# Kernel tuning notes

Hardware: AMD Instinct MI355X
Metric: run time of the kernel (lower is better)

The kernel has to match this reference:

```python
import jax, jax.numpy as jnp
import numpy as np

EPS = 1e-5

def _layer_norm(x, gamma, beta):
    mu = jnp.mean(x, axis=-1, keepdims=True)
    var = jnp.mean(jnp.square(x - mu), axis=-1, keepdims=True)
    return (x - mu) * jax.lax.rsqrt(var + EPS) * gamma + beta

def setup_inputs() -> dict:
    key = jax.random.key(0)
    ks = jax.random.split(key, 4)
    B, S, D, F = 4, 2048, 1024, 4096
    return {
        "hidden_state": jax.random.normal(ks[0], (B, S, D), dtype=jnp.float32),
        "attention_mask": jnp.zeros((B, S), dtype=jnp.float32),
        "w1": jax.random.normal(ks[1], (D, F), dtype=jnp.float32) * (1.0 / np.sqrt(D)),
        "b1": jnp.zeros((F,), dtype=jnp.float32),
        "w2": jax.random.normal(ks[2], (F, D), dtype=jnp.float32) * (1.0 / np.sqrt(F)),
        "b2": jnp.zeros((D,), dtype=jnp.float32),
        "ln1_gamma": jnp.ones((D,), dtype=jnp.float32),
        "ln1_beta": jnp.zeros((D,), dtype=jnp.float32),
        "ln2_gamma": jnp.ones((D,), dtype=jnp.float32),
        "ln2_beta": jnp.zeros((D,), dtype=jnp.float32),
    }

def reference(hidden_state, attention_mask, w1, b1, w2, b2,
              ln1_gamma, ln1_beta, ln2_gamma, ln2_beta):
    h = hidden_state
    d = h.shape[-1]
    # Self-attention with Q=K=V=h (no projections), single head.
    scores = jnp.einsum("bqd,bkd->bqk", h, h) / jnp.sqrt(jnp.float32(d))
    scores = scores + attention_mask[:, None, :]  # additive mask [B,1,S]
    probs = jax.nn.softmax(scores, axis=-1)
    attn_out = jnp.einsum("bqk,bkd->bqd", probs, h)
    # Residual + post-LN (dropout inactive in eval)
    h = _layer_norm(h + attn_out, ln1_gamma, ln1_beta)
    # FFN: Linear -> exact GELU -> Linear
    ffn = jax.nn.gelu(h @ w1 + b1, approximate=False) @ w2 + b2
    h = _layer_norm(h + ffn, ln2_gamma, ln2_beta)
    return h
```

## Files before the change

### kernel.cpp

```cpp
#include <hip/hip_runtime.h>
#include <hip/hip_bf16.h>
#include <math.h>

typedef __bf16 bf16;
typedef __bf16 bf16x8 __attribute__((ext_vector_type(8)));
typedef float  f32x4  __attribute__((ext_vector_type(4)));

__device__ __forceinline__ float gelu_f(float x) {
    return 0.5f * x * (1.0f + erff(x * 0.70710678118654752440f));
}

__global__ void detect_k(const unsigned short* __restrict__ h, int* __restrict__ flag)
{
    if (threadIdx.x == 0 && blockIdx.x == 0) {
        int cnt = 0;
        for (int i = 0; i < 256; i += 2) {
            int e = (h[i] >> 7) & 0xFF;
            cnt += (e >= 100 && e <= 140) ? 1 : 0;
        }
        *flag = (cnt >= 96) ? 0 : 1;
    }
}

struct SmallConvArgs {
    const void* src[7];
    bf16* dst[7];
    int n[7];
};
__global__ __launch_bounds__(256) void small_convert_k(SmallConvArgs a,
                                                       const int* __restrict__ flag)
{
    const int seg = blockIdx.y;
    const int i = blockIdx.x * 256 + threadIdx.x;
    if (i >= a.n[seg]) return;
    const float v = (*flag) ? ((const float*)a.src[seg])[i]
                            : (float)((const bf16*)a.src[seg])[i];
    a.dst[seg][i] = (bf16)v;
}

__global__ __launch_bounds__(256) void conv_transpose_k(
    const void* __restrict__ in, bf16* __restrict__ outT,
    int R, int C, const int* __restrict__ flag)
{
    __shared__ bf16 tile[32][33];
    const int c0 = blockIdx.x * 32;
    const int r0 = blockIdx.y * 32;
    const int tx = threadIdx.x & 31;
    const int ty = threadIdx.x >> 5;
    const bool f32 = (*flag) != 0;
#pragma unroll
    for (int i = 0; i < 32; i += 8) {
        const long idx = (long)(r0 + ty + i) * C + (c0 + tx);
        const float v = f32 ? ((const float*)in)[idx] : (float)((const bf16*)in)[idx];
        tile[ty + i][tx] = (bf16)v;
    }
    __syncthreads();
#pragma unroll
    for (int i = 0; i < 32; i += 8)
        outT[(long)(c0 + ty + i) * R + (r0 + tx)] = tile[tx][ty + i];
}

__global__ __launch_bounds__(256) void conv_transpose_h_k(
    const void* __restrict__ in, bf16* __restrict__ h_bf, bf16* __restrict__ hT,
    int S, int D, const int* __restrict__ flag)
{
    __shared__ bf16 tile[32][33];
    const long sB = (long)S * D;
    const int d0 = blockIdx.x * 32;
    const int s0 = blockIdx.y * 32;
    const int b  = blockIdx.z;
    const int tx = threadIdx.x & 31;
    const int ty = threadIdx.x >> 5;
    const bool f32 = (*flag) != 0;
#pragma unroll
    for (int i = 0; i < 32; i += 8) {
        const long idx = b * sB + (long)(s0 + ty + i) * D + (d0 + tx);
        const float v = f32 ? ((const float*)in)[idx] : (float)((const bf16*)in)[idx];
        const bf16 bv = (bf16)v;
        h_bf[idx] = bv;
        tile[ty + i][tx] = bv;
    }
    __syncthreads();
#pragma unroll
    for (int i = 0; i < 32; i += 8)
        hT[b * sB + (long)(d0 + ty + i) * S + (s0 + tx)] = tile[tx][ty + i];
}

__device__ __forceinline__ void gll16(const bf16* g, bf16* l)
{
    __builtin_amdgcn_global_load_lds(
        (const __attribute__((address_space(1))) void*)g,
        (__attribute__((address_space(3))) void*)l, 16, 0, 0);
}

template <int MODE, int STAGE>
__global__ __launch_bounds__(256) void gemm_nt(
    const bf16* __restrict__ A, const bf16* __restrict__ Bt,
    bf16* __restrict__ C, const bf16* __restrict__ bias,
    int M, int N, int K, float scale,
    long sA, long sB, long sC)
{
    A  += (long)blockIdx.z * sA;
    Bt += (long)blockIdx.z * sB;
    C  += (long)blockIdx.z * sC;

    const int tileM = blockIdx.y * 128;
    const int tileN = blockIdx.x * 128;

    const int t    = threadIdx.x;
    const int lane = t & 63;
    const int wave = t >> 6;
    const int wr   = wave >> 1;
    const int wc   = wave & 1;
    const int quad = lane >> 4;
    const int l16  = lane & 15;

    const int srow   = lane >> 3;
    const int lchunk = ((lane & 7) - srow) & 7;

    f32x4 acc[4][4] = {};

    auto swz = [](int row, int chunk) { return row * 64 + (((chunk + row) & 7) * 8); };

    auto stage = [&](bf16* as, bf16* bs, int k0) {
#pragma unroll
        for (int r2 = 0; r2 < 4; ++r2) {
            const int unit = wave * 4 + r2;
            const int row  = unit * 8 + srow;
            const int col  = lchunk * 8;
            gll16(A  + (long)(tileM + row) * K + (k0 + col), as + unit * 512);
            gll16(Bt + (long)(tileN + row) * K + (k0 + col), bs + unit * 512);
        }
    };

    auto compute = [&](const bf16* as, const bf16* bs) {
#pragma unroll
        for (int kk = 0; kk < 64; kk += 32) {
            const int chunk = (kk >> 3) + quad;
            bf16x8 af[4], bfr[4];
#pragma unroll
            for (int i = 0; i < 4; ++i) {
                af[i]  = *(const bf16x8*)&as[swz(wr * 64 + i * 16 + l16, chunk)];
                bfr[i] = *(const bf16x8*)&bs[swz(wc * 64 + i * 16 + l16, chunk)];
            }
#pragma unroll
            for (int mi = 0; mi < 4; ++mi)
#pragma unroll
                for (int ni = 0; ni < 4; ++ni)
                    acc[mi][ni] = __builtin_amdgcn_mfma_f32_16x16x32_bf16(
                        af[mi], bfr[ni], acc[mi][ni], 0, 0, 0);
        }
    };

    if constexpr (STAGE == 2) {
        __shared__ __align__(16) bf16 As0[128 * 64];
        __shared__ __align__(16) bf16 As1[128 * 64];
        __shared__ __align__(16) bf16 Bs0[128 * 64];
        __shared__ __align__(16) bf16 Bs1[128 * 64];

        stage(As0, Bs0, 0);
        __syncthreads();
        for (int u = 0; u < K / 64; u += 2) {
            const int k1 = (u + 1) * 64;
            const int k2 = (u + 2) * 64;
            if (k1 < K) stage(As1, Bs1, k1);
            compute(As0, Bs0);
            __syncthreads();
            if (k1 < K) {
                if (k2 < K) stage(As0, Bs0, k2);
                compute(As1, Bs1);
                __syncthreads();
            }
        }
    } else {
        __shared__ __align__(16) bf16 As[128 * 64];
        __shared__ __align__(16) bf16 Bs[128 * 64];
        for (int k0 = 0; k0 < K; k0 += 64) {
            stage(As, Bs, k0);
            __syncthreads();
            compute(As, Bs);
            __syncthreads();
        }
    }

#pragma unroll
    for (int mi = 0; mi < 4; ++mi) {
        const int rbase = tileM + wr * 64 + mi * 16 + quad * 4;
#pragma unroll
        for (int ni = 0; ni < 4; ++ni) {
            const int col = tileN + wc * 64 + ni * 16 + l16;
            float bv = 0.0f;
            if (MODE >= 2) bv = (float)bias[col];
#pragma unroll
            for (int r = 0; r < 4; ++r) {
                float v = acc[mi][ni][r];
                if (MODE == 0) v *= scale;
                if (MODE >= 2) v += bv;
                if (MODE == 2) v = gelu_f(v);
                C[(long)(rbase + r) * N + col] = (bf16)v;
            }
        }
    }
}

__global__ __launch_bounds__(256) void softmax_k(
    bf16* __restrict__ scores, const bf16* __restrict__ mask, int S)
{
    const long rowOff = ((long)blockIdx.y * S + blockIdx.x) * S;
    bf16* row = scores + rowOff;
    const bf16* mrow = mask + (long)blockIdx.y * S;
    const int t = threadIdx.x;

    const bf16x8 r = ((const bf16x8*)row)[t];
    const bf16x8 m = ((const bf16x8*)mrow)[t];
    float v[8];
    float mx = -1e30f;
#pragma unroll
    for (int i = 0; i < 8; ++i) {
        v[i] = (float)r[i] + (float)m[i];
        mx = fmaxf(mx, v[i]);
    }
#pragma unroll
    for (int off = 32; off > 0; off >>= 1)
        mx = fmaxf(mx, __shfl_down(mx, off));
    __shared__ float redm[4];
    if ((t & 63) == 0) redm[t >> 6] = mx;
    __syncthreads();
    mx = fmaxf(fmaxf(redm[0], redm[1]), fmaxf(redm[2], redm[3]));

    float s = 0.0f;
#pragma unroll
    for (int i = 0; i < 8; ++i) { v[i] = __expf(v[i] - mx); s += v[i]; }
#pragma unroll
    for (int off = 32; off > 0; off >>= 1)
        s += __shfl_down(s, off);
    __shared__ float reds[4];
    if ((t & 63) == 0) reds[t >> 6] = s;
    __syncthreads();
    s = reds[0] + reds[1] + reds[2] + reds[3];
    const float inv = 1.0f / s;
    bf16x8 o;
#pragma unroll
    for (int i = 0; i < 8; ++i) o[i] = (bf16)(v[i] * inv);
    ((bf16x8*)row)[t] = o;
}

__global__ __launch_bounds__(128) void ln_residual_k(
    const bf16* __restrict__ x1, const bf16* __restrict__ x2,
    const bf16* __restrict__ gamma, const bf16* __restrict__ beta,
    bf16* __restrict__ out)
{
    constexpr int D = 1024;
    const long off = (long)blockIdx.x * D;
    const int t = threadIdx.x;
    const bf16x8 a = ((const bf16x8*)(x1 + off))[t];
    const bf16x8 b = ((const bf16x8*)(x2 + off))[t];
    float v[8];
    float s = 0.0f, s2 = 0.0f;
#pragma unroll
    for (int i = 0; i < 8; ++i) {
        v[i] = (float)a[i] + (float)b[i];
        s  += v[i];
        s2 += v[i] * v[i];
    }
#pragma unroll
    for (int o2 = 32; o2 > 0; o2 >>= 1) {
        s  += __shfl_down(s, o2);
        s2 += __shfl_down(s2, o2);
    }
    __shared__ float rs[2], rs2[2];
    if ((t & 63) == 0) { rs[t >> 6] = s; rs2[t >> 6] = s2; }
    __syncthreads();
    s  = rs[0] + rs[1];
    s2 = rs2[0] + rs2[1];
    const float mean = s / (float)D;
    const float var  = s2 / (float)D - mean * mean;
    const float inv  = rsqrtf(var + 1e-5f);
    const bf16x8 g  = ((const bf16x8*)gamma)[t];
    const bf16x8 be = ((const bf16x8*)beta)[t];
    bf16x8 o;
#pragma unroll
    for (int i = 0; i < 8; ++i)
        o[i] = (bf16)((v[i] - mean) * inv * (float)g[i] + (float)be[i]);
    ((bf16x8*)(out + off))[t] = o;
}

__global__ __launch_bounds__(128) void ln_out_k(
    const bf16* __restrict__ x1, const bf16* __restrict__ x2,
    const bf16* __restrict__ gamma, const bf16* __restrict__ beta,
    void* __restrict__ outv, const int* __restrict__ flag)
{
    constexpr int D = 1024;
    const long off = (long)blockIdx.x * D;
    const int t = threadIdx.x;
    const bf16x8 a = ((const bf16x8*)(x1 + off))[t];
    const bf16x8 b = ((const bf16x8*)(x2 + off))[t];
    float v[8];
    float s = 0.0f, s2 = 0.0f;
#pragma unroll
    for (int i = 0; i < 8; ++i) {
        v[i] = (float)a[i] + (float)b[i];
        s  += v[i];
        s2 += v[i] * v[i];
    }
#pragma unroll
    for (int o2 = 32; o2 > 0; o2 >>= 1) {
        s  += __shfl_down(s, o2);
        s2 += __shfl_down(s2, o2);
    }
    __shared__ float rs[2], rs2[2];
    if ((t & 63) == 0) { rs[t >> 6] = s; rs2[t >> 6] = s2; }
    __syncthreads();
    s  = rs[0] + rs[1];
    s2 = rs2[0] + rs2[1];
    const float mean = s / (float)D;
    const float var  = s2 / (float)D - mean * mean;
    const float inv  = rsqrtf(var + 1e-5f);
    const bf16x8 g  = ((const bf16x8*)gamma)[t];
    const bf16x8 be = ((const bf16x8*)beta)[t];
    if (*flag) {
        f32x4 o1, o2v;
#pragma unroll
        for (int i = 0; i < 4; ++i) {
            o1[i]  = (v[i] - mean) * inv * (float)g[i] + (float)be[i];
            o2v[i] = (v[4 + i] - mean) * inv * (float)g[4 + i] + (float)be[4 + i];
        }
        f32x4* op = (f32x4*)((float*)outv + off);
        op[t * 2]     = o1;
        op[t * 2 + 1] = o2v;
    } else {
        bf16x8 o;
#pragma unroll
        for (int i = 0; i < 8; ++i)
            o[i] = (bf16)((v[i] - mean) * inv * (float)g[i] + (float)be[i]);
        ((bf16x8*)((bf16*)outv + off))[t] = o;
    }
}

extern "C" void kernel_launch(void* const* d_in, const int* in_sizes, int n_in,
                              void* d_out, int out_size, void* d_ws, size_t ws_size,
                              hipStream_t stream)
{
    constexpr int B = 4, S = 2048, D = 1024, F = 4096;
    constexpr long MB = 1024 * 1024;

    const void* h_raw  = d_in[0];
    const void* mk_raw = d_in[1];
    const void* w1_raw = d_in[2];
    const void* b1_raw = d_in[3];
    const void* w2_raw = d_in[4];
    const void* b2_raw = d_in[5];
    const void* g1_raw = d_in[6];
    const void* be1_raw= d_in[7];
    const void* g2_raw = d_in[8];
    const void* be2_raw= d_in[9];

    char* ws = (char*)d_ws;
    bf16* scores = (bf16*)(ws + 0);
    bf16* gact   = (bf16*)(ws + 0);
    bf16* hT     = (bf16*)(ws + 32 * MB);
    bf16* h_bf   = (bf16*)(ws + 48 * MB);
    bf16* y1     = (bf16*)(ws + 64 * MB);
    bf16* w1T    = (bf16*)(ws + 80 * MB);
    bf16* w2T    = (bf16*)(ws + 88 * MB);
    bf16* axf    = (bf16*)(ws + 96 * MB);
    char* sm     = ws + 112 * MB;
    int*  flag   = (int*)(sm);
    bf16* mk_bf  = (bf16*)(sm + 1024);
    bf16* b1_bf  = (bf16*)(sm + 17408 + 1024);
    bf16* b2_bf  = (bf16*)(sm + 25600 + 3072);
    bf16* g1_bf  = (bf16*)(sm + 27648 + 3072);
    bf16* be1_bf = (bf16*)(sm + 29696 + 3072);
    bf16* g2_bf  = (bf16*)(sm + 31744 + 3072);
    bf16* be2_bf = (bf16*)(sm + 33792 + 3072);

    const long SD = (long)S * D;
    const long SS = (long)S * S;

    detect_k<<<1, 64, 0, stream>>>((const unsigned short*)h_raw, flag);

    SmallConvArgs sca;
    sca.src[0] = mk_raw;  sca.dst[0] = mk_bf;  sca.n[0] = B * S;
    sca.src[1] = b1_raw;  sca.dst[1] = b1_bf;  sca.n[1] = F;
    sca.src[2] = b2_raw;  sca.dst[2] = b2_bf;  sca.n[2] = D;
    sca.src[3] = g1_raw;  sca.dst[3] = g1_bf;  sca.n[3] = D;
    sca.src[4] = be1_raw; sca.dst[4] = be1_bf; sca.n[4] = D;
    sca.src[5] = g2_raw;  sca.dst[5] = g2_bf;  sca.n[5] = D;
    sca.src[6] = be2_raw; sca.dst[6] = be2_bf; sca.n[6] = D;
    small_convert_k<<<dim3((B * S) / 256, 7), 256, 0, stream>>>(sca, flag);

    conv_transpose_h_k<<<dim3(D / 32, S / 32, B), 256, 0, stream>>>(
        h_raw, h_bf, hT, S, D, flag);

    conv_transpose_k<<<dim3(F / 32, D / 32), 256, 0, stream>>>(w1_raw, w1T, D, F, flag);
    conv_transpose_k<<<dim3(D / 32, F / 32), 256, 0, stream>>>(w2_raw, w2T, F, D, flag);

    gemm_nt<0, 2><<<dim3(S / 128, S / 128, B), 256, 0, stream>>>(
        h_bf, h_bf, scores, nullptr, S, S, D, 0.03125f, SD, SD, SS);

    softmax_k<<<dim3(S, B), 256, 0, stream>>>(scores, mk_bf, S);

    gemm_nt<1, 1><<<dim3(D / 128, S / 128, B), 256, 0, stream>>>(
        scores, hT, axf, nullptr, S, D, S, 1.0f, SS, SD, SD);

    ln_residual_k<<<B * S, 128, 0, stream>>>(h_bf, axf, g1_bf, be1_bf, y1);

    gemm_nt<2, 2><<<dim3(F / 128, (B * S) / 128, 1), 256, 0, stream>>>(
        y1, w1T, gact, b1_bf, B * S, F, D, 1.0f, 0, 0, 0);

    gemm_nt<3, 2><<<dim3(D / 128, (B * S) / 128, 1), 256, 0, stream>>>(
        gact, w2T, axf, b2_bf, B * S, D, F, 1.0f, 0, 0, 0);

    ln_out_k<<<B * S, 128, 0, stream>>>(y1, axf, g2_bf, be2_bf, d_out, flag);
}
```

Measured before the change: 450.4 us.

## Enlarge GEMM tiles to 256x256/256x128 with 8-wave blocks

Replaces the 128x128, 4-wave GEMM with a templated kernel using 256xBN block tiles and 512 threads (2x4 wave grid). The larger tiles raise arithmetic intensity per byte loaded into LDS and cut global traffic. All four GEMMs now use the double-buffered pipeline, including the P*V GEMM, which was single-buffered before. In exchange it uses more LDS (up to 128KB) and more accumulator registers per thread, which can limit occupancy and leaves fewer blocks for the smaller GEMMs, hurting wave-quantisation on the 256-CU part.

```diff
diff --git a/kernel.cpp b/kernel.cpp
--- a/kernel.cpp
+++ b/kernel.cpp
@@ -93,43 +93,57 @@
         (__attribute__((address_space(3))) void*)l, 16, 0, 0);
 }
 
-template <int MODE, int STAGE>
-__global__ __launch_bounds__(256) void gemm_nt(
+template <int MODE, int BM, int BN>
+__global__ __launch_bounds__(512, 2) void gemm_big(
     const bf16* __restrict__ A, const bf16* __restrict__ Bt,
     bf16* __restrict__ C, const bf16* __restrict__ bias,
     int M, int N, int K, float scale,
     long sA, long sB, long sC)
 {
+    constexpr int WM = BM / 2;
+    constexpr int WN = BN / 4;
+    constexpr int MI = WM / 16;
+    constexpr int NI = WN / 16;
+
     A  += (long)blockIdx.z * sA;
     Bt += (long)blockIdx.z * sB;
     C  += (long)blockIdx.z * sC;
 
-    const int tileM = blockIdx.y * 128;
-    const int tileN = blockIdx.x * 128;
+    const int tileM = blockIdx.y * BM;
+    const int tileN = blockIdx.x * BN;
+
+    __shared__ __align__(16) bf16 As0[BM * 64];
+    __shared__ __align__(16) bf16 As1[BM * 64];
+    __shared__ __align__(16) bf16 Bs0[BN * 64];
+    __shared__ __align__(16) bf16 Bs1[BN * 64];
 
     const int t    = threadIdx.x;
     const int lane = t & 63;
     const int wave = t >> 6;
-    const int wr   = wave >> 1;
-    const int wc   = wave & 1;
+    const int wr   = wave >> 2;
+    const int wc   = wave & 3;
     const int quad = lane >> 4;
     const int l16  = lane & 15;
 
     const int srow   = lane >> 3;
     const int lchunk = ((lane & 7) - srow) & 7;
 
-    f32x4 acc[4][4] = {};
+    f32x4 acc[MI][NI] = {};
 
     auto swz = [](int row, int chunk) { return row * 64 + (((chunk + row) & 7) * 8); };
 
     auto stage = [&](bf16* as, bf16* bs, int k0) {
 #pragma unroll
-        for (int r2 = 0; r2 < 4; ++r2) {
-            const int unit = wave * 4 + r2;
+        for (int r2 = 0; r2 < BM / 64; ++r2) {
+            const int unit = wave * (BM / 64) + r2;
             const int row  = unit * 8 + srow;
-            const int col  = lchunk * 8;
-            gll16(A  + (long)(tileM + row) * K + (k0 + col), as + unit * 512);
-            gll16(Bt + (long)(tileN + row) * K + (k0 + col), bs + unit * 512);
+            gll16(A + (long)(tileM + row) * K + (k0 + lchunk * 8), as + unit * 512);
+        }
+#pragma unroll
+        for (int r2 = 0; r2 < BN / 64; ++r2) {
+            const int unit = wave * (BN / 64) + r2;
+            const int row  = unit * 8 + srow;
+            gll16(Bt + (long)(tileN + row) * K + (k0 + lchunk * 8), bs + unit * 512);
         }
     };
 
@@ -137,58 +151,43 @@
 #pragma unroll
         for (int kk = 0; kk < 64; kk += 32) {
             const int chunk = (kk >> 3) + quad;
-            bf16x8 af[4], bfr[4];
-#pragma unroll
-            for (int i = 0; i < 4; ++i) {
-                af[i]  = *(const bf16x8*)&as[swz(wr * 64 + i * 16 + l16, chunk)];
-                bfr[i] = *(const bf16x8*)&bs[swz(wc * 64 + i * 16 + l16, chunk)];
-            }
-#pragma unroll
-            for (int mi = 0; mi < 4; ++mi)
-#pragma unroll
-                for (int ni = 0; ni < 4; ++ni)
+            bf16x8 af[MI], bfr[NI];
+#pragma unroll
+            for (int i = 0; i < MI; ++i)
+                af[i] = *(const bf16x8*)&as[swz(wr * WM + i * 16 + l16, chunk)];
+#pragma unroll
+            for (int j = 0; j < NI; ++j)
+                bfr[j] = *(const bf16x8*)&bs[swz(wc * WN + j * 16 + l16, chunk)];
+#pragma unroll
+            for (int mi = 0; mi < MI; ++mi)
+#pragma unroll
+                for (int ni = 0; ni < NI; ++ni)
                     acc[mi][ni] = __builtin_amdgcn_mfma_f32_16x16x32_bf16(
                         af[mi], bfr[ni], acc[mi][ni], 0, 0, 0);
         }
     };
 
-    if constexpr (STAGE == 2) {
-        __shared__ __align__(16) bf16 As0[128 * 64];
-        __shared__ __align__(16) bf16 As1[128 * 64];
-        __shared__ __align__(16) bf16 Bs0[128 * 64];
-        __shared__ __align__(16) bf16 Bs1[128 * 64];
-
-        stage(As0, Bs0, 0);
+    stage(As0, Bs0, 0);
+    __syncthreads();
+    for (int u = 0; u < K / 64; u += 2) {
+        const int k1 = (u + 1) * 64;
+        const int k2 = (u + 2) * 64;
+        if (k1 < K) stage(As1, Bs1, k1);
+        compute(As0, Bs0);
         __syncthreads();
-        for (int u = 0; u < K / 64; u += 2) {
-            const int k1 = (u + 1) * 64;
-            const int k2 = (u + 2) * 64;
-            if (k1 < K) stage(As1, Bs1, k1);
-            compute(As0, Bs0);
+        if (k1 < K) {
+            if (k2 < K) stage(As0, Bs0, k2);
+            compute(As1, Bs1);
             __syncthreads();
-            if (k1 < K) {
-                if (k2 < K) stage(As0, Bs0, k2);
-                compute(As1, Bs1);
-                __syncthreads();
-            }
-        }
-    } else {
-        __shared__ __align__(16) bf16 As[128 * 64];
-        __shared__ __align__(16) bf16 Bs[128 * 64];
-        for (int k0 = 0; k0 < K; k0 += 64) {
-            stage(As, Bs, k0);
-            __syncthreads();
-            compute(As, Bs);
-            __syncthreads();
-        }
-    }
-
-#pragma unroll
-    for (int mi = 0; mi < 4; ++mi) {
-        const int rbase = tileM + wr * 64 + mi * 16 + quad * 4;
-#pragma unroll
-        for (int ni = 0; ni < 4; ++ni) {
-            const int col = tileN + wc * 64 + ni * 16 + l16;
+        }
+    }
+
+#pragma unroll
+    for (int mi = 0; mi < MI; ++mi) {
+        const int rbase = tileM + wr * WM + mi * 16 + quad * 4;
+#pragma unroll
+        for (int ni = 0; ni < NI; ++ni) {
+            const int col = tileN + wc * WN + ni * 16 + l16;
             float bv = 0.0f;
             if (MODE >= 2) bv = (float)bias[col];
 #pragma unroll
@@ -395,20 +394,20 @@
     conv_transpose_k<<<dim3(F / 32, D / 32), 256, 0, stream>>>(w1_raw, w1T, D, F, flag);
     conv_transpose_k<<<dim3(D / 32, F / 32), 256, 0, stream>>>(w2_raw, w2T, F, D, flag);
 
-    gemm_nt<0, 2><<<dim3(S / 128, S / 128, B), 256, 0, stream>>>(
+    gemm_big<0, 256, 256><<<dim3(S / 256, S / 256, B), 512, 0, stream>>>(
         h_bf, h_bf, scores, nullptr, S, S, D, 0.03125f, SD, SD, SS);
 
     softmax_k<<<dim3(S, B), 256, 0, stream>>>(scores, mk_bf, S);
 
-    gemm_nt<1, 1><<<dim3(D / 128, S / 128, B), 256, 0, stream>>>(
+    gemm_big<1, 256, 128><<<dim3(D / 128, S / 256, B), 512, 0, stream>>>(
         scores, hT, axf, nullptr, S, D, S, 1.0f, SS, SD, SD);
 
     ln_residual_k<<<B * S, 128, 0, stream>>>(h_bf, axf, g1_bf, be1_bf, y1);
 
-    gemm_nt<2, 2><<<dim3(F / 128, (B * S) / 128, 1), 256, 0, stream>>>(
+    gemm_big<2, 256, 256><<<dim3(F / 256, (B * S) / 256, 1), 512, 0, stream>>>(
         y1, w1T, gact, b1_bf, B * S, F, D, 1.0f, 0, 0, 0);
 
-    gemm_nt<3, 2><<<dim3(D / 128, (B * S) / 128, 1), 256, 0, stream>>>(
+    gemm_big<3, 256, 128><<<dim3(D / 128, (B * S) / 256, 1), 512, 0, stream>>>(
         gact, w2T, axf, b2_bf, B * S, D, F, 1.0f, 0, 0, 0);
 
     ln_out_k<<<B * S, 128, 0, stream>>>(y1, axf, g2_bf, be2_bf, d_out, flag);
```

Result: no change. 443.1 us (-1.6%).
